# Kernel optimization log

Measured on AMD Instinct MI355X. Metric: run time of the kernel, lower is better.

## Reference

```python
import jax, jax.numpy as jnp
import numpy as np

N, E, B = 50000, 1000000, 64
IN, HID, OUT, H, ED = 25, 128, 64, 4, 6
EPS = 1e-5


def gat_layer(x, src, dst, ea, W, att_s, att_d, We, att_e, bias, heads, ch):
    """PyG GATConv with edge features and self-loops (fill_value='mean').
    x: [N,F_in]; src,dst: [E'] (after self-loops); ea: [E',ED]."""
    n = x.shape[0]
    h = (x @ W).reshape(n, heads, ch)                    # [N,H,C]
    a_src = jnp.einsum('nhc,hc->nh', h, att_s)           # [N,H]
    a_dst = jnp.einsum('nhc,hc->nh', h, att_d)
    e = (ea @ We).reshape(-1, heads, ch)                 # [E',H,C]
    a_edge = jnp.einsum('ehc,hc->eh', e, att_e)          # [E',H]
    alpha = a_src[src] + a_dst[dst] + a_edge
    alpha = jax.nn.leaky_relu(alpha, 0.2)
    # segment softmax over incoming edges of each dst node
    amax = jax.ops.segment_max(alpha, dst, num_segments=n)
    alpha = jnp.exp(alpha - amax[dst])
    denom = jax.ops.segment_sum(alpha, dst, num_segments=n)
    alpha = alpha / (denom[dst] + 1e-16)
    msg = h[src] * alpha[..., None]                      # [E',H,C]
    out = jax.ops.segment_sum(msg, dst, num_segments=n)
    return out.reshape(n, heads * ch) + bias


def batch_norm(x, g, b):
    mu = x.mean(0)
    var = x.var(0)
    return (x - mu) * jax.lax.rsqrt(var + EPS) * g + b


def setup_inputs():
    key = jax.random.key(0)
    ks = jax.random.split(key, 32)
    s = 0.1
    inp = {
        'x': jax.random.normal(ks[0], (N, IN), jnp.float32),
        'edge_index': jax.random.randint(ks[1], (2, E), 0, N, jnp.int32),
        'edge_attr': jax.random.uniform(ks[2], (E, ED), jnp.float32),
        'batch': jnp.sort(jax.random.randint(ks[3], (N,), 0, B, jnp.int32)),
        'repeat_unit_mask': jax.random.randint(ks[4], (N,), 0, 3, jnp.int32),
        'num_graphs': B,
        # layer 1: 25 -> 4 heads x 32
        'W1': jax.random.normal(ks[5], (IN, HID)) * s,
        'att_s1': jax.random.normal(ks[6], (H, HID // H)) * s,
        'att_d1': jax.random.normal(ks[7], (H, HID // H)) * s,
        'We1': jax.random.normal(ks[8], (ED, HID)) * s,
        'att_e1': jax.random.normal(ks[9], (H, HID // H)) * s,
        'b1': jnp.zeros((HID,)),
        'g1': jnp.ones((HID,)), 'be1': jnp.zeros((HID,)),
        # layer 2: 128 -> 4 heads x 32
        'W2': jax.random.normal(ks[10], (HID, HID)) * s,
        'att_s2': jax.random.normal(ks[11], (H, HID // H)) * s,
        'att_d2': jax.random.normal(ks[12], (H, HID // H)) * s,
        'We2': jax.random.normal(ks[13], (ED, HID)) * s,
        'att_e2': jax.random.normal(ks[14], (H, HID // H)) * s,
        'b2': jnp.zeros((HID,)),
        'g2': jnp.ones((HID,)), 'be2': jnp.zeros((HID,)),
        # layer 3: 128 -> 1 head x 64
        'W3': jax.random.normal(ks[15], (HID, OUT)) * s,
        'att_s3': jax.random.normal(ks[16], (1, OUT)) * s,
        'att_d3': jax.random.normal(ks[17], (1, OUT)) * s,
        'We3': jax.random.normal(ks[18], (ED, OUT)) * s,
        'att_e3': jax.random.normal(ks[19], (1, OUT)) * s,
        'b3': jnp.zeros((OUT,)),
    }
    return inp


def reference(x, edge_index, edge_attr, batch, repeat_unit_mask, num_graphs,
              W1, att_s1, att_d1, We1, att_e1, b1, g1, be1,
              W2, att_s2, att_d2, We2, att_e2, b2, g2, be2,
              W3, att_s3, att_d3, We3, att_e3, b3):
    n = x.shape[0]
    # add self-loops once (shared by all layers), edge_attr fill = mean
    loop = jnp.arange(n, dtype=edge_index.dtype)
    src = jnp.concatenate([edge_index[0], loop])
    dst = jnp.concatenate([edge_index[1], loop])
    ea = jnp.concatenate([edge_attr, jnp.broadcast_to(edge_attr.mean(0), (n, edge_attr.shape[1]))], 0)

    h = gat_layer(x, src, dst, ea, W1, att_s1, att_d1, We1, att_e1, b1, H, HID // H)
    h = jax.nn.elu(batch_norm(h, g1, be1))               # dropout = identity (eval)
    h = gat_layer(h, src, dst, ea, W2, att_s2, att_d2, We2, att_e2, b2, H, HID // H)
    h = jax.nn.elu(batch_norm(h, g2, be2))
    h = gat_layer(h, src, dst, ea, W3, att_s3, att_d3, We3, att_e3, b3, 1, OUT)
    h = jax.nn.elu(h)                                    # [N, OUT]

    # GRIN pooling: max over middle repeat-unit atoms (mask == 1) per graph
    mid = (repeat_unit_mask == 1)
    vals = jnp.where(mid[:, None], h, -jnp.inf)
    out = jax.ops.segment_max(vals, batch, num_segments=num_graphs)
    out = jnp.where(jnp.isfinite(out), out, 0.0)         # empty segments -> 0 (torch_scatter default)
    return out
```

## Files before the change

kernel.cpp:

```cpp
#include <hip/hip_runtime.h>
#include <hip/hip_bf16.h>
#include <cstdint>


typedef __attribute__((ext_vector_type(8))) short short8;
typedef __attribute__((ext_vector_type(4))) float floatx4;

__device__ __forceinline__ void atomicMaxFloat(float* addr, float val) {
  if (val >= 0.f) atomicMax((int*)addr, __float_as_int(val));
  else            atomicMin((unsigned int*)addr, __float_as_uint(val));
}

__device__ __forceinline__ float bf2f(unsigned short u) {
  union { uint32_t i; float f; } v; v.i = ((uint32_t)u) << 16; return v.f;
}
__device__ __forceinline__ float u2f(uint32_t u) {
  union { uint32_t i; float f; } v; v.i = u; return v.f;
}
__device__ __forceinline__ unsigned short f2bf(float f) {
  return __bfloat16_as_ushort(__float2bfloat16(f));
}
__device__ __forceinline__ uint32_t pk2(float a, float b) {
  return (uint32_t)f2bf(a) | ((uint32_t)f2bf(b) << 16);
}

#define EA_NBLK 256
#define PCH 4096

__global__ __launch_bounds__(256) void ea_count_kernel(
    const float* __restrict__ ea, float* __restrict__ ea_part,
    const int* __restrict__ dst, int* __restrict__ part,
    int E, int EP, int CB) {
  if (blockIdx.x < EA_NBLK) {
    const int bid = blockIdx.x;
    const int total = 6 * E;
    const int total12 = total / 12;
    float a0 = 0.f, a1 = 0.f, a2 = 0.f, a3 = 0.f, a4 = 0.f, a5 = 0.f;
    const int stride = EA_NBLK * 256;
    for (int i = bid * 256 + threadIdx.x; i < total12; i += stride) {
      const float* b = ea + (size_t)i * 12;
      float4 f0 = *reinterpret_cast<const float4*>(b);
      float4 f1 = *reinterpret_cast<const float4*>(b + 4);
      float4 f2 = *reinterpret_cast<const float4*>(b + 8);
      a0 += f0.x + f1.z;
      a1 += f0.y + f1.w;
      a2 += f0.z + f2.x;
      a3 += f0.w + f2.y;
      a4 += f1.x + f2.z;
      a5 += f1.y + f2.w;
    }
    if (bid == 0 && threadIdx.x == 0) {
      for (int i = total12 * 12; i < total; ++i) {
        int c = i % 6;
        float v = ea[i];
        a0 += (c == 0) ? v : 0.f;
        a1 += (c == 1) ? v : 0.f;
        a2 += (c == 2) ? v : 0.f;
        a3 += (c == 3) ? v : 0.f;
        a4 += (c == 4) ? v : 0.f;
        a5 += (c == 5) ? v : 0.f;
      }
    }
#pragma unroll
    for (int mm = 32; mm >= 1; mm >>= 1) {
      a0 += __shfl_xor(a0, mm); a1 += __shfl_xor(a1, mm);
      a2 += __shfl_xor(a2, mm); a3 += __shfl_xor(a3, mm);
      a4 += __shfl_xor(a4, mm); a5 += __shfl_xor(a5, mm);
    }
    __shared__ float ls[4][6];
    const int lane = threadIdx.x & 63, wv = threadIdx.x >> 6;
    if (lane == 0) {
      ls[wv][0] = a0; ls[wv][1] = a1; ls[wv][2] = a2;
      ls[wv][3] = a3; ls[wv][4] = a4; ls[wv][5] = a5;
    }
    __syncthreads();
    if (threadIdx.x < 6) {
      float s = ls[0][threadIdx.x] + ls[1][threadIdx.x] +
                ls[2][threadIdx.x] + ls[3][threadIdx.x];
      ea_part[threadIdx.x * EA_NBLK + bid] = s;
    }
  } else {
    const int bid = blockIdx.x - EA_NBLK;
    __shared__ int lcnt[256];
    lcnt[threadIdx.x] = 0;
    __syncthreads();
    const int g0 = bid * PCH + threadIdx.x;
#pragma unroll
    for (int j = 0; j < 16; ++j) {
      int g = g0 + j * 256;
      if (g < EP) {
        int d = (g < E) ? dst[g] : (g - E);
        atomicAdd(&lcnt[d >> 8], 1);
      }
    }
    __syncthreads();
    part[(size_t)bid * 256 + threadIdx.x] = lcnt[threadIdx.x];
  }
}

__global__ __launch_bounds__(384) void prep_kernel(
    const float* __restrict__ part, float invE,
    const float* __restrict__ We1, const float* __restrict__ ae1,
    const float* __restrict__ We2, const float* __restrict__ ae2,
    const float* __restrict__ We3, const float* __restrict__ ae3,
    float* __restrict__ we_red, float* __restrict__ ea_mean6) {
  const int tid = threadIdx.x;
  {
    const int ch = tid >> 6, lane = tid & 63;
    float s = part[ch * EA_NBLK + lane] + part[ch * EA_NBLK + lane + 64] +
              part[ch * EA_NBLK + lane + 128] + part[ch * EA_NBLK + lane + 192];
#pragma unroll
    for (int mm = 32; mm >= 1; mm >>= 1) s += __shfl_xor(s, mm);
    if (lane == 0) ea_mean6[ch] = s * invE;
  }
  for (int idx = tid; idx < 72; idx += 384) {
    int l = idx / 24, rem = idx % 24, k = rem / 4, h = rem % 4;
    const float* We; const float* ae; int C, HEADS, F_OUT;
    if (l == 0)      { We = We1; ae = ae1; C = 32; HEADS = 4; F_OUT = 128; }
    else if (l == 1) { We = We2; ae = ae2; C = 32; HEADS = 4; F_OUT = 128; }
    else             { We = We3; ae = ae3; C = 64; HEADS = 1; F_OUT = 64;  }
    float s = 0.f;
    if (h < HEADS)
      for (int c = 0; c < C; ++c) s += We[k * F_OUT + h * C + c] * ae[h * C + c];
    we_red[idx] = s;
  }
}

__global__ __launch_bounds__(256) void bin_scan_kernel(
    int* __restrict__ part, int* __restrict__ btot, int CB, int NB) {
  const int c = blockIdx.x;
  const int tid = threadIdx.x, lane = tid & 63, wv = tid >> 6;
  const int K = (NB + 255) / 256;
  int vals[4];
  int s = 0;
#pragma unroll 4
  for (int k = 0; k < K; ++k) {
    int b = tid * K + k;
    vals[k] = (b < NB) ? part[(size_t)b * 256 + c] : 0;
    s += vals[k];
  }
  int x = s;
#pragma unroll
  for (int off = 1; off < 64; off <<= 1) {
    int t = __shfl_up(x, off);
    if (lane >= off) x += t;
  }
  __shared__ int ws[4];
  if (lane == 63) ws[wv] = x;
  __syncthreads();
  int woff = 0;
#pragma unroll
  for (int k = 0; k < 3; ++k) woff += (k < wv) ? ws[k] : 0;
  int run = woff + x - s;
#pragma unroll 4
  for (int k = 0; k < K; ++k) {
    int b = tid * K + k;
    if (b < NB) part[(size_t)b * 256 + c] = run;
    run += vals[k];
  }
  if (tid == 255) btot[c] = woff + x;
}

__global__ __launch_bounds__(256) void cbase_scan_kernel(
    const int* __restrict__ btot, int* __restrict__ cbase, int CB) {
  const int c = threadIdx.x, lane = c & 63, wv = c >> 6;
  int t = (c < CB) ? btot[c] : 0;
  int x = t;
#pragma unroll
  for (int off = 1; off < 64; off <<= 1) {
    int u = __shfl_up(x, off);
    if (lane >= off) x += u;
  }
  __shared__ int ws[4];
  if (lane == 63) ws[wv] = x;
  __syncthreads();
  int woff = 0;
#pragma unroll
  for (int k = 0; k < 3; ++k) woff += (k < wv) ? ws[k] : 0;
  const int excl = woff + x - t;
  if (c < CB) cbase[c] = excl;
  if (c == CB - 1) cbase[CB] = excl + t;
}

__global__ __launch_bounds__(256) void partition_kernel(
    const int* __restrict__ src, const int* __restrict__ dst,
    const float* __restrict__ ea, const float* __restrict__ ea_mean6,
    const int* __restrict__ part, const int* __restrict__ cbase,
    uint4* __restrict__ ev_tmp, int E, int EP, int CB) {
  __shared__ int loff[256];
  __shared__ int lrk[256];
  lrk[threadIdx.x] = 0;
  if (threadIdx.x < CB)
    loff[threadIdx.x] = cbase[threadIdx.x] +
                        part[(size_t)blockIdx.x * 256 + threadIdx.x];
  __syncthreads();
  const int g0 = blockIdx.x * PCH + threadIdx.x;
#pragma unroll
  for (int j = 0; j < 16; ++j) {
    int g = g0 + j * 256;
    if (g >= EP) continue;
    int d, s;
    float e0, e1, e2, e3, e4, e5;
    if (g < E) {
      d = dst[g]; s = src[g];
      const float* r = ea + (size_t)g * 6;
      float2 f0 = *reinterpret_cast<const float2*>(r);
      float2 f1 = *reinterpret_cast<const float2*>(r + 2);
      float2 f2 = *reinterpret_cast<const float2*>(r + 4);
      e0 = f0.x; e1 = f0.y; e2 = f1.x; e3 = f1.y; e4 = f2.x; e5 = f2.y;
    } else {
      d = g - E; s = d;
      e0 = ea_mean6[0]; e1 = ea_mean6[1]; e2 = ea_mean6[2];
      e3 = ea_mean6[3]; e4 = ea_mean6[4]; e5 = ea_mean6[5];
    }
    const int c = d >> 8;
    const int lr = atomicAdd(&lrk[c], 1);
    uint4 o;
    o.x = (uint32_t)s | ((uint32_t)d << 16);
    o.y = pk2(e0, e1);
    o.z = pk2(e2, e3);
    o.w = pk2(e4, e5);
    ev_tmp[loff[c] + lr] = o;
  }
}

__global__ __launch_bounds__(512) void fine_csr_kernel(
    const uint4* __restrict__ ev_tmp, const int* __restrict__ cbase,
    uint4* __restrict__ ev, int* __restrict__ row_ptr,
    int nN, int CB, int EP) {
  __shared__ int lcnt[256];
  __shared__ int lexcl[256];
  __shared__ int lrk[256];
  __shared__ int ws[4];
  const int tid = threadIdx.x;
  const int c = blockIdx.x;
  if (tid < 256) { lcnt[tid] = 0; lrk[tid] = 0; }
  __syncthreads();
  const int e0 = cbase[c], e1 = cbase[c + 1];
  for (int p = e0 + tid; p < e1; p += 512) {
    uint4 e = ev_tmp[p];
    atomicAdd(&lcnt[(e.x >> 16) & 255], 1);
  }
  __syncthreads();
  const int lane = tid & 63, wv = tid >> 6;
  int v = 0, x = 0;
  if (tid < 256) {
    v = lcnt[tid];
    x = v;
#pragma unroll
    for (int off = 1; off < 64; off <<= 1) {
      int t = __shfl_up(x, off);
      if (lane >= off) x += t;
    }
    if (lane == 63) ws[wv] = x;
  }
  __syncthreads();
  if (tid < 256) {
    int woff = 0;
#pragma unroll
    for (int k = 0; k < 3; ++k) woff += (k < wv) ? ws[k] : 0;
    const int ex = woff + x - v;
    lexcl[tid] = ex;
    const int node = (c << 8) + tid;
    if (node < nN) row_ptr[node] = e0 + ex;
    if (c == CB - 1 && tid == 0) row_ptr[nN] = EP;
  }
  __syncthreads();
  for (int p = e0 + tid; p < e1; p += 512) {
    uint4 e = ev_tmp[p];
    const int li = (int)((e.x >> 16) & 255);
    const int pos = e0 + lexcl[li] + atomicAdd(&lrk[li], 1);
    ev[pos] = e;
  }
}

__global__ __launch_bounds__(256) void pack_conv_kernel(
    const float* __restrict__ W1, const float* __restrict__ W2,
    const float* __restrict__ W3, __hip_bfloat16* __restrict__ wp,
    const float* __restrict__ x, __hip_bfloat16* __restrict__ xb, int nN) {
  int idx = blockIdx.x * 256 + threadIdx.x;
  if (idx < 28672) {
    const float* W; int F_IN, F_OUT, KC, rem;
    if (idx < 4096)       { W = W1; F_IN = 25;  F_OUT = 128; KC = 1; rem = idx; }
    else if (idx < 20480) { W = W2; F_IN = 128; F_OUT = 128; KC = 4; rem = idx - 4096; }
    else                  { W = W3; F_IN = 128; F_OUT = 64;  KC = 4; rem = idx - 20480; }
    int ct = rem / (KC * 512);
    int r2 = rem % (KC * 512);
    int kc = r2 / 512;
    int li = r2 % 512;
    int lane = li >> 3, j = li & 7;
    int k = kc * 32 + ((lane >> 4) << 3) + j;
    int col = ct * 16 + (lane & 15);
    float v = (k < F_IN) ? W[(size_t)k * F_OUT + col] : 0.f;
    wp[idx] = __float2bfloat16(v);
  } else {
    int i = idx - 28672;
    if (i < nN * 32) {
      int n = i >> 5, k = i & 31;
      xb[i] = __float2bfloat16(k < 25 ? x[(size_t)n * 25 + k] : 0.f);
    }
  }
}

#define BN_NBLK 256
__global__ __launch_bounds__(256) void bn_stats_kernel(
    const __hip_bfloat16* __restrict__ x, float* __restrict__ part, int nN) {
  const int c8 = threadIdx.x & 15;
  const int slot = threadIdx.x >> 4;
  float s[8], s2[8];
#pragma unroll
  for (int j = 0; j < 8; ++j) { s[j] = 0.f; s2[j] = 0.f; }
  for (int n = blockIdx.x * 16 + slot; n < nN; n += BN_NBLK * 16) {
    short8 v = *reinterpret_cast<const short8*>(x + (size_t)n * 128 + c8 * 8);
#pragma unroll
    for (int j = 0; j < 8; ++j) {
      float f = bf2f((unsigned short)v[j]);
      s[j] += f; s2[j] += f * f;
    }
  }
#pragma unroll
  for (int j = 0; j < 8; ++j) {
    s[j]  += __shfl_xor(s[j], 16);  s[j]  += __shfl_xor(s[j], 32);
    s2[j] += __shfl_xor(s2[j], 16); s2[j] += __shfl_xor(s2[j], 32);
  }
  __shared__ float ls[4][256];
  const int lane = threadIdx.x & 63, wv = threadIdx.x >> 6;
  if (lane < 16) {
#pragma unroll
    for (int j = 0; j < 8; ++j) {
      ls[wv][c8 * 8 + j] = s[j];
      ls[wv][128 + c8 * 8 + j] = s2[j];
    }
  }
  __syncthreads();
  const int i = threadIdx.x;
  part[(size_t)blockIdx.x * 256 + i] = ls[0][i] + ls[1][i] + ls[2][i] + ls[3][i];
}

__global__ __launch_bounds__(256) void bn_finalize_kernel(
    const float* __restrict__ part,
    const float* __restrict__ g, const float* __restrict__ b,
    float* __restrict__ scale, float* __restrict__ shift, float invN) {
  const int i = threadIdx.x;
  float v0 = 0.f, v1 = 0.f, v2 = 0.f, v3 = 0.f;
  for (int bk = 0; bk < BN_NBLK; bk += 4) {
    v0 += part[(size_t)bk * 256 + i];
    v1 += part[(size_t)(bk + 1) * 256 + i];
    v2 += part[(size_t)(bk + 2) * 256 + i];
    v3 += part[(size_t)(bk + 3) * 256 + i];
  }
  __shared__ float sums[256];
  sums[i] = (v0 + v1) + (v2 + v3);
  __syncthreads();
  if (i < 128) {
    float mu = sums[i] * invN;
    float var = sums[128 + i] * invN - mu * mu;
    float sc = rsqrtf(var + 1e-5f) * g[i];
    scale[i] = sc;
    shift[i] = b[i] - mu * sc;
  }
}

template<int K, int NT, int KC, int HEADS, bool BN>
__global__ __launch_bounds__(256) void feat_mfma_kernel(
    const void* __restrict__ xin, const __hip_bfloat16* __restrict__ wp,
    const float* __restrict__ att_s, const float* __restrict__ att_d,
    const float* __restrict__ bsc, const float* __restrict__ bsh,
    __hip_bfloat16* __restrict__ hout, float* __restrict__ a_src,
    float* __restrict__ a_dst, int nN) {
  constexpr int F_OUT = NT * 16;
  __shared__ __hip_bfloat16 hs[64][F_OUT + 4];
  const int tid = threadIdx.x;
  const int lane = tid & 63, w = tid >> 6;
  const int base = blockIdx.x * 64;

  const int nd = min(base + (w << 4) + (lane & 15), nN - 1);
  short8 a[KC];
  if constexpr (!BN) {
    const __hip_bfloat16* xb = (const __hip_bfloat16*)xin;
#pragma unroll
    for (int kc = 0; kc < KC; ++kc)
      a[kc] = *reinterpret_cast<const short8*>(
          xb + (size_t)nd * K + kc * 32 + ((lane >> 4) << 3));
  } else {
    const __hip_bfloat16* xb = (const __hip_bfloat16*)xin;
#pragma unroll
    for (int kc = 0; kc < KC; ++kc) {
      const int kb = kc * 32 + ((lane >> 4) << 3);
      short8 xv = *reinterpret_cast<const short8*>(xb + (size_t)nd * K + kb);
      float4 s0 = *reinterpret_cast<const float4*>(bsc + kb);
      float4 s1 = *reinterpret_cast<const float4*>(bsc + kb + 4);
      float4 t0 = *reinterpret_cast<const float4*>(bsh + kb);
      float4 t1 = *reinterpret_cast<const float4*>(bsh + kb + 4);
      float scj[8] = {s0.x, s0.y, s0.z, s0.w, s1.x, s1.y, s1.z, s1.w};
      float shj[8] = {t0.x, t0.y, t0.z, t0.w, t1.x, t1.y, t1.z, t1.w};
      union { short8 sv; unsigned short us[8]; } u;
#pragma unroll
      for (int j = 0; j < 8; ++j) {
        float v = bf2f((unsigned short)xv[j]) * scj[j] + shj[j];
        float t = (v > 0.f) ? v : (__expf(v) - 1.f);
        u.us[j] = f2bf(t);
      }
      a[kc] = u.sv;
    }
  }

  floatx4 acc[NT];
#pragma unroll
  for (int ct = 0; ct < NT; ++ct) acc[ct] = (floatx4){0.f, 0.f, 0.f, 0.f};

#pragma unroll
  for (int ct = 0; ct < NT; ++ct) {
#pragma unroll
    for (int kc = 0; kc < KC; ++kc) {
      short8 b = *reinterpret_cast<const short8*>(wp + ((size_t)(ct * KC + kc) * 64 + lane) * 8);
      acc[ct] = __builtin_amdgcn_mfma_f32_16x16x32_bf16(a[kc], b, acc[ct], 0, 0, 0);
    }
  }

#pragma unroll
  for (int ct = 0; ct < NT; ++ct) {
#pragma unroll
    for (int r = 0; r < 4; ++r) {
      int row = (w << 4) + ((lane >> 4) << 2) + r;
      hs[row][ct * 16 + (lane & 15)] = __float2bfloat16(acc[ct][r]);
    }
  }
  __syncthreads();

  {
    constexpr int PART = F_OUT / 4;
    const int ln = tid >> 2, q = tid & 3;
    const int n = base + ln;
    float ssum = 0.f, dsum = 0.f;
#pragma unroll
    for (int j = 0; j < PART; ++j) {
      int c = q * PART + j;
      float hv = bf2f(__bfloat16_as_ushort(hs[ln][c]));
      ssum += hv * att_s[c];
      dsum += hv * att_d[c];
    }
    if constexpr (HEADS == 4) {
      if (n < nN) {
        a_src[(size_t)n * 4 + q] = ssum;
        a_dst[(size_t)n * 4 + q] = dsum;
      }
    } else {
      ssum += __shfl_xor(ssum, 1); ssum += __shfl_xor(ssum, 2);
      dsum += __shfl_xor(dsum, 1); dsum += __shfl_xor(dsum, 2);
      if (n < nN && q == 0) { a_src[n] = ssum; a_dst[n] = dsum; }
    }
  }

  constexpr int C4 = F_OUT / 4;
  for (int idx = tid; idx < 64 * C4; idx += 256) {
    int row = idx / C4, cw = idx % C4;
    int n = base + row;
    if (n < nN)
      *reinterpret_cast<uint2*>(hout + (size_t)n * F_OUT + cw * 4) =
          *reinterpret_cast<const uint2*>(&hs[row][cw * 4]);
  }
}

template<int HEADS, int C>
__global__ __launch_bounds__(256) void agg_kernel(
    const int* __restrict__ row_ptr, const uint4* __restrict__ ev,
    const float* __restrict__ we_red,
    const float* __restrict__ a_src, const float* __restrict__ a_dst,
    const __hip_bfloat16* __restrict__ hfeat,
    const float* __restrict__ bias, __hip_bfloat16* __restrict__ out, int nN) {
  const int lane = threadIdx.x & 63;
  const int n = blockIdx.x * 4 + (threadIdx.x >> 6);
  if (n >= nN) return;
  const int r0 = row_ptr[n], r1 = row_ptr[n + 1];

#define FMA2(k, ha, hb)                                                   \
  acc2[k].x += wA * u2f((ha) << 16) + wB * u2f((hb) << 16);               \
  acc2[k].y += wA * u2f((ha) & 0xffff0000u) + wB * u2f((hb) & 0xffff0000u);

  if constexpr (HEADS == 4) {
    const int es = lane >> 4;
    const int L = lane & 15;
    const int fo = L << 3;
    const int h = L >> 2;
    const int q1 = L & 1;
    const float wr0 = we_red[0 * 4 + h], wr1 = we_red[1 * 4 + h];
    const float wr2 = we_red[2 * 4 + h], wr3 = we_red[3 * 4 + h];
    const float wr4 = we_red[4 * 4 + h], wr5 = we_red[5 * 4 + h];
    const float adh = a_dst[(size_t)n * 4 + h];
    float2 acc2[4];
#pragma unroll
    for (int j = 0; j < 4; ++j) acc2[j] = make_float2(0.f, 0.f);
    float dsum = 0.f;
    int p = r0 + es;
    uint4 wa = make_uint4(0, 0, 0, 0), wb = make_uint4(0, 0, 0, 0);
    if (p < r1) wa = ev[p];
    if (p + 4 < r1) wb = ev[p + 4];
    for (; p < r1; p += 8) {
      const int sA = (int)(wa.x & 0xffffu);
      const int sB = (int)(wb.x & 0xffffu);
      uint4 hA = *reinterpret_cast<const uint4*>(hfeat + (size_t)sA * 128 + fo);
      uint4 hB = *reinterpret_cast<const uint4*>(hfeat + (size_t)sB * 128 + fo);
      const uint32_t ry = q1 ? wb.y : wa.y;
      const uint32_t rz = q1 ? wb.z : wa.z;
      const uint32_t rw = q1 ? wb.w : wa.w;
      const int ss = q1 ? sB : sA;
      const float asS = a_src[(size_t)ss * 4 + h];
      const int pn = p + 8;
      uint4 wa_n = make_uint4(0, 0, 0, 0), wb_n = make_uint4(0, 0, 0, 0);
      if (pn < r1) wa_n = ev[pn];
      if (pn + 4 < r1) wb_n = ev[pn + 4];
      float ae = u2f(ry << 16) * wr0 + u2f(ry & 0xffff0000u) * wr1 +
                 u2f(rz << 16) * wr2 + u2f(rz & 0xffff0000u) * wr3 +
                 u2f(rw << 16) * wr4 + u2f(rw & 0xffff0000u) * wr5;
      float a = asS + adh + ae;
      a = (a >= 0.f) ? a : 0.2f * a;
      const float wme = __expf(a);
      const float wot = __shfl_xor(wme, 1);
      const float wA = q1 ? wot : wme;
      float wB = q1 ? wme : wot;
      wB = (p + 4 < r1) ? wB : 0.f;
      dsum += wA + wB;
      FMA2(0, hA.x, hB.x); FMA2(1, hA.y, hB.y);
      FMA2(2, hA.z, hB.z); FMA2(3, hA.w, hB.w);
      wa = wa_n; wb = wb_n;
    }
#pragma unroll
    for (int j = 0; j < 4; ++j) {
      acc2[j].x += __shfl_xor(acc2[j].x, 16);
      acc2[j].y += __shfl_xor(acc2[j].y, 16);
      acc2[j].x += __shfl_xor(acc2[j].x, 32);
      acc2[j].y += __shfl_xor(acc2[j].y, 32);
    }
    dsum += __shfl_xor(dsum, 16);
    dsum += __shfl_xor(dsum, 32);
    if (lane < 16) {
      const float invd = 1.f / (dsum + 1e-16f);
      float4 b0 = *reinterpret_cast<const float4*>(bias + fo);
      float4 b1 = *reinterpret_cast<const float4*>(bias + fo + 4);
      uint4 o;
      o.x = pk2(acc2[0].x * invd + b0.x, acc2[0].y * invd + b0.y);
      o.y = pk2(acc2[1].x * invd + b0.z, acc2[1].y * invd + b0.w);
      o.z = pk2(acc2[2].x * invd + b1.x, acc2[2].y * invd + b1.y);
      o.w = pk2(acc2[3].x * invd + b1.z, acc2[3].y * invd + b1.w);
      *reinterpret_cast<uint4*>(out + (size_t)n * 128 + fo) = o;
    }
  } else {
    const int es = lane >> 3;
    const int L = lane & 7;
    const int fo = L << 3;
    const int q1 = L & 1;
    const float wr0 = we_red[0], wr1 = we_red[4], wr2 = we_red[8];
    const float wr3 = we_red[12], wr4 = we_red[16], wr5 = we_red[20];
    const float adh = a_dst[n];
    float2 acc2[4];
#pragma unroll
    for (int j = 0; j < 4; ++j) acc2[j] = make_float2(0.f, 0.f);
    float dsum = 0.f;
    int p = r0 + es;
    uint4 wa = make_uint4(0, 0, 0, 0), wb = make_uint4(0, 0, 0, 0);
    if (p < r1) wa = ev[p];
    if (p + 8 < r1) wb = ev[p + 8];
    for (; p < r1; p += 16) {
      const int sA = (int)(wa.x & 0xffffu);
      const int sB = (int)(wb.x & 0xffffu);
      uint4 hA = *reinterpret_cast<const uint4*>(hfeat + (size_t)sA * 64 + fo);
      uint4 hB = *reinterpret_cast<const uint4*>(hfeat + (size_t)sB * 64 + fo);
      const uint32_t ry = q1 ? wb.y : wa.y;
      const uint32_t rz = q1 ? wb.z : wa.z;
      const uint32_t rw = q1 ? wb.w : wa.w;
      const int ss = q1 ? sB : sA;
      const float asS = a_src[ss];
      const int pn = p + 16;
      uint4 wa_n = make_uint4(0, 0, 0, 0), wb_n = make_uint4(0, 0, 0, 0);
      if (pn < r1) wa_n = ev[pn];
      if (pn + 8 < r1) wb_n = ev[pn + 8];
      float ae = u2f(ry << 16) * wr0 + u2f(ry & 0xffff0000u) * wr1 +
                 u2f(rz << 16) * wr2 + u2f(rz & 0xffff0000u) * wr3 +
                 u2f(rw << 16) * wr4 + u2f(rw & 0xffff0000u) * wr5;
      float a = asS + adh + ae;
      a = (a >= 0.f) ? a : 0.2f * a;
      const float wme = __expf(a);
      const float wot = __shfl_xor(wme, 1);
      const float wA = q1 ? wot : wme;
      float wB = q1 ? wme : wot;
      wB = (p + 8 < r1) ? wB : 0.f;
      dsum += wA + wB;
      FMA2(0, hA.x, hB.x); FMA2(1, hA.y, hB.y);
      FMA2(2, hA.z, hB.z); FMA2(3, hA.w, hB.w);
      wa = wa_n; wb = wb_n;
    }
#pragma unroll
    for (int j = 0; j < 4; ++j) {
      acc2[j].x += __shfl_xor(acc2[j].x, 8);
      acc2[j].y += __shfl_xor(acc2[j].y, 8);
      acc2[j].x += __shfl_xor(acc2[j].x, 16);
      acc2[j].y += __shfl_xor(acc2[j].y, 16);
      acc2[j].x += __shfl_xor(acc2[j].x, 32);
      acc2[j].y += __shfl_xor(acc2[j].y, 32);
    }
    dsum += __shfl_xor(dsum, 8);
    dsum += __shfl_xor(dsum, 16);
    dsum += __shfl_xor(dsum, 32);
    if (lane < 8) {
      const float invd = 1.f / (dsum + 1e-16f);
      float4 b0 = *reinterpret_cast<const float4*>(bias + fo);
      float4 b1 = *reinterpret_cast<const float4*>(bias + fo + 4);
      uint4 o;
      o.x = pk2(acc2[0].x * invd + b0.x, acc2[0].y * invd + b0.y);
      o.y = pk2(acc2[1].x * invd + b0.z, acc2[1].y * invd + b0.w);
      o.z = pk2(acc2[2].x * invd + b1.x, acc2[2].y * invd + b1.y);
      o.w = pk2(acc2[3].x * invd + b1.z, acc2[3].y * invd + b1.w);
      *reinterpret_cast<uint4*>(out + (size_t)n * 64 + fo) = o;
    }
  }
#undef FMA2
}

__global__ __launch_bounds__(64) void pool_kernel(
    const __hip_bfloat16* __restrict__ h3, const int* __restrict__ batch,
    const int* __restrict__ mask, float* __restrict__ out, int nN) {
  const int c = threadIdx.x;
  int n0 = blockIdx.x * 32;
  int n1 = min(n0 + 32, nN);
  float cur = -INFINITY;
  int curb = -1;
  for (int n = n0; n < n1; ++n) {
    if (mask[n] != 1) continue;
    int b = batch[n];
    if (b != curb) {
      if (curb >= 0) atomicMaxFloat(&out[curb * 64 + c], cur);
      curb = b; cur = -INFINITY;
    }
    float v = bf2f(__bfloat16_as_ushort(h3[(size_t)n * 64 + c]));
    v = (v > 0.f) ? v : (__expf(v) - 1.f);
    cur = fmaxf(cur, v);
  }
  if (curb >= 0) atomicMaxFloat(&out[curb * 64 + c], cur);
}

__global__ __launch_bounds__(256) void fixup_kernel(float* __restrict__ out, int sz) {
  int i = blockIdx.x * 256 + threadIdx.x;
  if (i >= sz) return;
  float v = out[i];
  if (!(v > -INFINITY && v < INFINITY)) out[i] = 0.f;
}

extern "C" void kernel_launch(void* const* d_in, const int* in_sizes, int n_in,
                              void* d_out, int out_size, void* d_ws, size_t ws_size,
                              hipStream_t stream) {
  (void)n_in; (void)ws_size;
  const float* x     = (const float*)d_in[0];
  const int*   ei    = (const int*)d_in[1];
  const float* ea    = (const float*)d_in[2];
  const int*   batch = (const int*)d_in[3];
  const int*   mask  = (const int*)d_in[4];
  const float* W1 = (const float*)d_in[6];
  const float* as1 = (const float*)d_in[7];
  const float* ad1 = (const float*)d_in[8];
  const float* We1 = (const float*)d_in[9];
  const float* ae1 = (const float*)d_in[10];
  const float* b1 = (const float*)d_in[11];
  const float* g1 = (const float*)d_in[12];
  const float* be1 = (const float*)d_in[13];
  const float* W2 = (const float*)d_in[14];
  const float* as2 = (const float*)d_in[15];
  const float* ad2 = (const float*)d_in[16];
  const float* We2 = (const float*)d_in[17];
  const float* ae2 = (const float*)d_in[18];
  const float* b2 = (const float*)d_in[19];
  const float* g2 = (const float*)d_in[20];
  const float* be2 = (const float*)d_in[21];
  const float* W3 = (const float*)d_in[22];
  const float* as3 = (const float*)d_in[23];
  const float* ad3 = (const float*)d_in[24];
  const float* We3 = (const float*)d_in[25];
  const float* ae3 = (const float*)d_in[26];
  const float* b3 = (const float*)d_in[27];

  const int N = in_sizes[0] / 25;
  const int E = in_sizes[1] / 2;
  const int EP = E + N;
  const int* srcI = ei;
  const int* dstI = ei + E;

  const int CB = (N + 255) >> 8;
  const int nb = (EP + PCH - 1) / PCH;

  char* w = (char*)d_ws;
  auto alloc = [&](size_t bytes) { char* p = w; w += (bytes + 255) / 256 * 256; return p; };
  float* ea_part = (float*)alloc(6 * EA_NBLK * 4);
  float* we_red  = (float*)alloc(3 * 6 * 4 * 4);
  float* ea_m6   = (float*)alloc(6 * 4);
  int*   row_ptr = (int*)alloc((size_t)(N + 1) * 4);
  int*   part    = (int*)alloc((size_t)nb * 256 * 4);
  int*   btot    = (int*)alloc((size_t)CB * 4);
  int*   cbase   = (int*)alloc((size_t)(CB + 1) * 4);
  uint4* ev      = (uint4*)alloc((size_t)EP * 16);
  float* a_srcb  = (float*)alloc((size_t)N * 4 * 4);
  float* a_dstb  = (float*)alloc((size_t)N * 4 * 4);
  __hip_bfloat16* hbuf = (__hip_bfloat16*)alloc((size_t)N * 128 * 2);
  size_t obsz = (size_t)N * 128 * 2;
  size_t evsz = (size_t)EP * 16;
  __hip_bfloat16* obuf = (__hip_bfloat16*)alloc(obsz > evsz ? obsz : evsz);
  __hip_bfloat16* x1b  = (__hip_bfloat16*)alloc((size_t)N * 32 * 2);
  __hip_bfloat16* wp   = (__hip_bfloat16*)alloc(28672 * 2);
  float* bn_part = (float*)alloc((size_t)BN_NBLK * 256 * 4);
  float* bn_sc   = (float*)alloc(128 * 4);
  float* bn_sh   = (float*)alloc(128 * 4);
  uint4* ev_tmp  = (uint4*)obuf;

  hipMemsetAsync(d_out, 0xFF, (size_t)out_size * 4, stream);
  ea_count_kernel<<<EA_NBLK + nb, 256, 0, stream>>>(ea, ea_part, dstI, part, E, EP, CB);
  prep_kernel<<<1, 384, 0, stream>>>(ea_part, 1.f / (float)E, We1, ae1, We2, ae2, We3, ae3,
                                     we_red, ea_m6);
  bin_scan_kernel<<<CB, 256, 0, stream>>>(part, btot, CB, nb);
  cbase_scan_kernel<<<1, 256, 0, stream>>>(btot, cbase, CB);
  partition_kernel<<<nb, 256, 0, stream>>>(srcI, dstI, ea, ea_m6, part, cbase,
                                           ev_tmp, E, EP, CB);
  fine_csr_kernel<<<CB, 512, 0, stream>>>(ev_tmp, cbase, ev, row_ptr, N, CB, EP);
  pack_conv_kernel<<<(28672 + N * 32 + 255) / 256, 256, 0, stream>>>(
      W1, W2, W3, wp, x, x1b, N);

  const int gMf = (N + 63) / 64;
  const int gAgg = (N + 3) / 4;

  feat_mfma_kernel<32, 8, 1, 4, false><<<gMf, 256, 0, stream>>>(
      x1b, wp, as1, ad1, nullptr, nullptr, hbuf, a_srcb, a_dstb, N);
  agg_kernel<4, 32><<<gAgg, 256, 0, stream>>>(row_ptr, ev, we_red + 0,
                                              a_srcb, a_dstb, hbuf, b1, obuf, N);
  bn_stats_kernel<<<BN_NBLK, 256, 0, stream>>>(obuf, bn_part, N);
  bn_finalize_kernel<<<1, 256, 0, stream>>>(bn_part, g1, be1, bn_sc, bn_sh, 1.f / (float)N);

  feat_mfma_kernel<128, 8, 4, 4, true><<<gMf, 256, 0, stream>>>(
      obuf, wp + 4096, as2, ad2, bn_sc, bn_sh, hbuf, a_srcb, a_dstb, N);
  agg_kernel<4, 32><<<gAgg, 256, 0, stream>>>(row_ptr, ev, we_red + 24,
                                              a_srcb, a_dstb, hbuf, b2, obuf, N);
  bn_stats_kernel<<<BN_NBLK, 256, 0, stream>>>(obuf, bn_part, N);
  bn_finalize_kernel<<<1, 256, 0, stream>>>(bn_part, g2, be2, bn_sc, bn_sh, 1.f / (float)N);

  feat_mfma_kernel<128, 4, 4, 1, true><<<gMf, 256, 0, stream>>>(
      obuf, wp + 20480, as3, ad3, bn_sc, bn_sh, hbuf, a_srcb, a_dstb, N);
  agg_kernel<1, 64><<<gAgg, 256, 0, stream>>>(row_ptr, ev, we_red + 48,
                                              a_srcb, a_dstb, hbuf, b3, obuf, N);

  pool_kernel<<<(N + 31) / 32, 64, 0, stream>>>(obuf, batch, mask, (float*)d_out, N);
  fixup_kernel<<<(out_size + 255) / 256, 256, 0, stream>>>((float*)d_out, out_size);
}
```

Before: 249.4 us.

## Split 4-head aggregation into two feature-half slices with interleaved block mapping

The 4-head aggregation kernel now splits each node's 128-wide feature row into two 64-wide slices handled by separate blocks. Blocks are interleaved so that both slices of the same node group run close together in time. Each wave uses 8 lanes per edge and 8 edges in flight, like the single-head path. The aim is to raise edge-level parallelism per wave and shrink the gathered footprint per block to improve cache locality. The cost is that edge records, a_src lookups and the exp/softmax work are repeated for each slice, doubling that part of the traffic.

```diff
diff --git a/kernel.cpp b/kernel.cpp
--- a/kernel.cpp
+++ b/kernel.cpp
@@ -462,8 +462,99 @@
   }
 }
 
-template<int HEADS, int C>
-__global__ __launch_bounds__(256) void agg_kernel(
+#define FMA2(k, ha, hb)                                                   \
+  acc2[k].x += wA * u2f((ha) << 16) + wB * u2f((hb) << 16);               \
+  acc2[k].y += wA * u2f((ha) & 0xffff0000u) + wB * u2f((hb) & 0xffff0000u);
+
+__global__ __launch_bounds__(256) void agg4s_kernel(
+    const int* __restrict__ row_ptr, const uint4* __restrict__ ev,
+    const float* __restrict__ we_red,
+    const float* __restrict__ a_src, const float* __restrict__ a_dst,
+    const __hip_bfloat16* __restrict__ hfeat,
+    const float* __restrict__ bias, __hip_bfloat16* __restrict__ out,
+    int nN, int ng) {
+  const int bid = blockIdx.x;
+  const int r = bid & 7, g = bid >> 3;
+  const int slice = r >> 2;
+  const int grp = g * 4 + (r & 3);
+  if (grp >= ng) return;
+  const int lane = threadIdx.x & 63;
+  const int n = grp * 4 + (threadIdx.x >> 6);
+  if (n >= nN) return;
+  const int r0 = row_ptr[n], r1 = row_ptr[n + 1];
+
+  const int es = lane >> 3;
+  const int L = lane & 7;
+  const int fo = slice * 64 + (L << 3);
+  const int h = fo >> 5;
+  const int q1 = L & 1;
+  const float wr0 = we_red[0 * 4 + h], wr1 = we_red[1 * 4 + h];
+  const float wr2 = we_red[2 * 4 + h], wr3 = we_red[3 * 4 + h];
+  const float wr4 = we_red[4 * 4 + h], wr5 = we_red[5 * 4 + h];
+  const float adh = a_dst[(size_t)n * 4 + h];
+  float2 acc2[4];
+#pragma unroll
+  for (int j = 0; j < 4; ++j) acc2[j] = make_float2(0.f, 0.f);
+  float dsum = 0.f;
+  int p = r0 + es;
+  uint4 wa = make_uint4(0, 0, 0, 0), wb = make_uint4(0, 0, 0, 0);
+  if (p < r1) wa = ev[p];
+  if (p + 8 < r1) wb = ev[p + 8];
+  for (; p < r1; p += 16) {
+    const int sA = (int)(wa.x & 0xffffu);
+    const int sB = (int)(wb.x & 0xffffu);
+    uint4 hA = *reinterpret_cast<const uint4*>(hfeat + (size_t)sA * 128 + fo);
+    uint4 hB = *reinterpret_cast<const uint4*>(hfeat + (size_t)sB * 128 + fo);
+    const uint32_t ry = q1 ? wb.y : wa.y;
+    const uint32_t rz = q1 ? wb.z : wa.z;
+    const uint32_t rw = q1 ? wb.w : wa.w;
+    const int ss = q1 ? sB : sA;
+    const float asS = a_src[(size_t)ss * 4 + h];
+    const int pn = p + 16;
+    uint4 wa_n = make_uint4(0, 0, 0, 0), wb_n = make_uint4(0, 0, 0, 0);
+    if (pn < r1) wa_n = ev[pn];
+    if (pn + 8 < r1) wb_n = ev[pn + 8];
+    float ae = u2f(ry << 16) * wr0 + u2f(ry & 0xffff0000u) * wr1 +
+               u2f(rz << 16) * wr2 + u2f(rz & 0xffff0000u) * wr3 +
+               u2f(rw << 16) * wr4 + u2f(rw & 0xffff0000u) * wr5;
+    float a = asS + adh + ae;
+    a = (a >= 0.f) ? a : 0.2f * a;
+    const float wme = __expf(a);
+    const float wot = __shfl_xor(wme, 1);
+    const float wA = q1 ? wot : wme;
+    float wB = q1 ? wme : wot;
+    wB = (p + 8 < r1) ? wB : 0.f;
+    dsum += wA + wB;
+    FMA2(0, hA.x, hB.x); FMA2(1, hA.y, hB.y);
+    FMA2(2, hA.z, hB.z); FMA2(3, hA.w, hB.w);
+    wa = wa_n; wb = wb_n;
+  }
+#pragma unroll
+  for (int j = 0; j < 4; ++j) {
+    acc2[j].x += __shfl_xor(acc2[j].x, 8);
+    acc2[j].y += __shfl_xor(acc2[j].y, 8);
+    acc2[j].x += __shfl_xor(acc2[j].x, 16);
+    acc2[j].y += __shfl_xor(acc2[j].y, 16);
+    acc2[j].x += __shfl_xor(acc2[j].x, 32);
+    acc2[j].y += __shfl_xor(acc2[j].y, 32);
+  }
+  dsum += __shfl_xor(dsum, 8);
+  dsum += __shfl_xor(dsum, 16);
+  dsum += __shfl_xor(dsum, 32);
+  if (lane < 8) {
+    const float invd = 1.f / (dsum + 1e-16f);
+    float4 b0 = *reinterpret_cast<const float4*>(bias + fo);
+    float4 b1 = *reinterpret_cast<const float4*>(bias + fo + 4);
+    uint4 o;
+    o.x = pk2(acc2[0].x * invd + b0.x, acc2[0].y * invd + b0.y);
+    o.y = pk2(acc2[1].x * invd + b0.z, acc2[1].y * invd + b0.w);
+    o.z = pk2(acc2[2].x * invd + b1.x, acc2[2].y * invd + b1.y);
+    o.w = pk2(acc2[3].x * invd + b1.z, acc2[3].y * invd + b1.w);
+    *reinterpret_cast<uint4*>(out + (size_t)n * 128 + fo) = o;
+  }
+}
+
+__global__ __launch_bounds__(256) void agg1_kernel(
     const int* __restrict__ row_ptr, const uint4* __restrict__ ev,
     const float* __restrict__ we_red,
     const float* __restrict__ a_src, const float* __restrict__ a_dst,
@@ -474,148 +565,75 @@
   if (n >= nN) return;
   const int r0 = row_ptr[n], r1 = row_ptr[n + 1];
 
-#define FMA2(k, ha, hb)                                                   \
-  acc2[k].x += wA * u2f((ha) << 16) + wB * u2f((hb) << 16);               \
-  acc2[k].y += wA * u2f((ha) & 0xffff0000u) + wB * u2f((hb) & 0xffff0000u);
-
-  if constexpr (HEADS == 4) {
-    const int es = lane >> 4;
-    const int L = lane & 15;
-    const int fo = L << 3;
-    const int h = L >> 2;
-    const int q1 = L & 1;
-    const float wr0 = we_red[0 * 4 + h], wr1 = we_red[1 * 4 + h];
-    const float wr2 = we_red[2 * 4 + h], wr3 = we_red[3 * 4 + h];
-    const float wr4 = we_red[4 * 4 + h], wr5 = we_red[5 * 4 + h];
-    const float adh = a_dst[(size_t)n * 4 + h];
-    float2 acc2[4];
-#pragma unroll
-    for (int j = 0; j < 4; ++j) acc2[j] = make_float2(0.f, 0.f);
-    float dsum = 0.f;
-    int p = r0 + es;
-    uint4 wa = make_uint4(0, 0, 0, 0), wb = make_uint4(0, 0, 0, 0);
-    if (p < r1) wa = ev[p];
-    if (p + 4 < r1) wb = ev[p + 4];
-    for (; p < r1; p += 8) {
-      const int sA = (int)(wa.x & 0xffffu);
-      const int sB = (int)(wb.x & 0xffffu);
-      uint4 hA = *reinterpret_cast<const uint4*>(hfeat + (size_t)sA * 128 + fo);
-      uint4 hB = *reinterpret_cast<const uint4*>(hfeat + (size_t)sB * 128 + fo);
-      const uint32_t ry = q1 ? wb.y : wa.y;
-      const uint32_t rz = q1 ? wb.z : wa.z;
-      const uint32_t rw = q1 ? wb.w : wa.w;
-      const int ss = q1 ? sB : sA;
-      const float asS = a_src[(size_t)ss * 4 + h];
-      const int pn = p + 8;
-      uint4 wa_n = make_uint4(0, 0, 0, 0), wb_n = make_uint4(0, 0, 0, 0);
-      if (pn < r1) wa_n = ev[pn];
-      if (pn + 4 < r1) wb_n = ev[pn + 4];
-      float ae = u2f(ry << 16) * wr0 + u2f(ry & 0xffff0000u) * wr1 +
-                 u2f(rz << 16) * wr2 + u2f(rz & 0xffff0000u) * wr3 +
-                 u2f(rw << 16) * wr4 + u2f(rw & 0xffff0000u) * wr5;
-      float a = asS + adh + ae;
-      a = (a >= 0.f) ? a : 0.2f * a;
-      const float wme = __expf(a);
-      const float wot = __shfl_xor(wme, 1);
-      const float wA = q1 ? wot : wme;
-      float wB = q1 ? wme : wot;
-      wB = (p + 4 < r1) ? wB : 0.f;
-      dsum += wA + wB;
-      FMA2(0, hA.x, hB.x); FMA2(1, hA.y, hB.y);
-      FMA2(2, hA.z, hB.z); FMA2(3, hA.w, hB.w);
-      wa = wa_n; wb = wb_n;
-    }
-#pragma unroll
-    for (int j = 0; j < 4; ++j) {
-      acc2[j].x += __shfl_xor(acc2[j].x, 16);
-      acc2[j].y += __shfl_xor(acc2[j].y, 16);
-      acc2[j].x += __shfl_xor(acc2[j].x, 32);
-      acc2[j].y += __shfl_xor(acc2[j].y, 32);
-    }
-    dsum += __shfl_xor(dsum, 16);
-    dsum += __shfl_xor(dsum, 32);
-    if (lane < 16) {
-      const float invd = 1.f / (dsum + 1e-16f);
-      float4 b0 = *reinterpret_cast<const float4*>(bias + fo);
-      float4 b1 = *reinterpret_cast<const float4*>(bias + fo + 4);
-      uint4 o;
-      o.x = pk2(acc2[0].x * invd + b0.x, acc2[0].y * invd + b0.y);
-      o.y = pk2(acc2[1].x * invd + b0.z, acc2[1].y * invd + b0.w);
-      o.z = pk2(acc2[2].x * invd + b1.x, acc2[2].y * invd + b1.y);
-      o.w = pk2(acc2[3].x * invd + b1.z, acc2[3].y * invd + b1.w);
-      *reinterpret_cast<uint4*>(out + (size_t)n * 128 + fo) = o;
-    }
-  } else {
-    const int es = lane >> 3;
-    const int L = lane & 7;
-    const int fo = L << 3;
-    const int q1 = L & 1;
-    const float wr0 = we_red[0], wr1 = we_red[4], wr2 = we_red[8];
-    const float wr3 = we_red[12], wr4 = we_red[16], wr5 = we_red[20];
-    const float adh = a_dst[n];
-    float2 acc2[4];
-#pragma unroll
-    for (int j = 0; j < 4; ++j) acc2[j] = make_float2(0.f, 0.f);
-    float dsum = 0.f;
-    int p = r0 + es;
-    uint4 wa = make_uint4(0, 0, 0, 0), wb = make_uint4(0, 0, 0, 0);
-    if (p < r1) wa = ev[p];
-    if (p + 8 < r1) wb = ev[p + 8];
-    for (; p < r1; p += 16) {
-      const int sA = (int)(wa.x & 0xffffu);
-      const int sB = (int)(wb.x & 0xffffu);
-      uint4 hA = *reinterpret_cast<const uint4*>(hfeat + (size_t)sA * 64 + fo);
-      uint4 hB = *reinterpret_cast<const uint4*>(hfeat + (size_t)sB * 64 + fo);
-      const uint32_t ry = q1 ? wb.y : wa.y;
-      const uint32_t rz = q1 ? wb.z : wa.z;
-      const uint32_t rw = q1 ? wb.w : wa.w;
-      const int ss = q1 ? sB : sA;
-      const float asS = a_src[ss];
-      const int pn = p + 16;
-      uint4 wa_n = make_uint4(0, 0, 0, 0), wb_n = make_uint4(0, 0, 0, 0);
-      if (pn < r1) wa_n = ev[pn];
-      if (pn + 8 < r1) wb_n = ev[pn + 8];
-      float ae = u2f(ry << 16) * wr0 + u2f(ry & 0xffff0000u) * wr1 +
-                 u2f(rz << 16) * wr2 + u2f(rz & 0xffff0000u) * wr3 +
-                 u2f(rw << 16) * wr4 + u2f(rw & 0xffff0000u) * wr5;
-      float a = asS + adh + ae;
-      a = (a >= 0.f) ? a : 0.2f * a;
-      const float wme = __expf(a);
-      const float wot = __shfl_xor(wme, 1);
-      const float wA = q1 ? wot : wme;
-      float wB = q1 ? wme : wot;
-      wB = (p + 8 < r1) ? wB : 0.f;
-      dsum += wA + wB;
-      FMA2(0, hA.x, hB.x); FMA2(1, hA.y, hB.y);
-      FMA2(2, hA.z, hB.z); FMA2(3, hA.w, hB.w);
-      wa = wa_n; wb = wb_n;
-    }
-#pragma unroll
-    for (int j = 0; j < 4; ++j) {
-      acc2[j].x += __shfl_xor(acc2[j].x, 8);
-      acc2[j].y += __shfl_xor(acc2[j].y, 8);
-      acc2[j].x += __shfl_xor(acc2[j].x, 16);
-      acc2[j].y += __shfl_xor(acc2[j].y, 16);
-      acc2[j].x += __shfl_xor(acc2[j].x, 32);
-      acc2[j].y += __shfl_xor(acc2[j].y, 32);
-    }
-    dsum += __shfl_xor(dsum, 8);
-    dsum += __shfl_xor(dsum, 16);
-    dsum += __shfl_xor(dsum, 32);
-    if (lane < 8) {
-      const float invd = 1.f / (dsum + 1e-16f);
-      float4 b0 = *reinterpret_cast<const float4*>(bias + fo);
-      float4 b1 = *reinterpret_cast<const float4*>(bias + fo + 4);
-      uint4 o;
-      o.x = pk2(acc2[0].x * invd + b0.x, acc2[0].y * invd + b0.y);
-      o.y = pk2(acc2[1].x * invd + b0.z, acc2[1].y * invd + b0.w);
-      o.z = pk2(acc2[2].x * invd + b1.x, acc2[2].y * invd + b1.y);
-      o.w = pk2(acc2[3].x * invd + b1.z, acc2[3].y * invd + b1.w);
-      *reinterpret_cast<uint4*>(out + (size_t)n * 64 + fo) = o;
-    }
-  }
+  const int es = lane >> 3;
+  const int L = lane & 7;
+  const int fo = L << 3;
+  const int q1 = L & 1;
+  const float wr0 = we_red[0], wr1 = we_red[4], wr2 = we_red[8];
+  const float wr3 = we_red[12], wr4 = we_red[16], wr5 = we_red[20];
+  const float adh = a_dst[n];
+  float2 acc2[4];
+#pragma unroll
+  for (int j = 0; j < 4; ++j) acc2[j] = make_float2(0.f, 0.f);
+  float dsum = 0.f;
+  int p = r0 + es;
+  uint4 wa = make_uint4(0, 0, 0, 0), wb = make_uint4(0, 0, 0, 0);
+  if (p < r1) wa = ev[p];
+  if (p + 8 < r1) wb = ev[p + 8];
+  for (; p < r1; p += 16) {
+    const int sA = (int)(wa.x & 0xffffu);
+    const int sB = (int)(wb.x & 0xffffu);
+    uint4 hA = *reinterpret_cast<const uint4*>(hfeat + (size_t)sA * 64 + fo);
+    uint4 hB = *reinterpret_cast<const uint4*>(hfeat + (size_t)sB * 64 + fo);
+    const uint32_t ry = q1 ? wb.y : wa.y;
+    const uint32_t rz = q1 ? wb.z : wa.z;
+    const uint32_t rw = q1 ? wb.w : wa.w;
+    const int ss = q1 ? sB : sA;
+    const float asS = a_src[ss];
+    const int pn = p + 16;
+    uint4 wa_n = make_uint4(0, 0, 0, 0), wb_n = make_uint4(0, 0, 0, 0);
+    if (pn < r1) wa_n = ev[pn];
+    if (pn + 8 < r1) wb_n = ev[pn + 8];
+    float ae = u2f(ry << 16) * wr0 + u2f(ry & 0xffff0000u) * wr1 +
+               u2f(rz << 16) * wr2 + u2f(rz & 0xffff0000u) * wr3 +
+               u2f(rw << 16) * wr4 + u2f(rw & 0xffff0000u) * wr5;
+    float a = asS + adh + ae;
+    a = (a >= 0.f) ? a : 0.2f * a;
+    const float wme = __expf(a);
+    const float wot = __shfl_xor(wme, 1);
+    const float wA = q1 ? wot : wme;
+    float wB = q1 ? wme : wot;
+    wB = (p + 8 < r1) ? wB : 0.f;
+    dsum += wA + wB;
+    FMA2(0, hA.x, hB.x); FMA2(1, hA.y, hB.y);
+    FMA2(2, hA.z, hB.z); FMA2(3, hA.w, hB.w);
+    wa = wa_n; wb = wb_n;
+  }
+#pragma unroll
+  for (int j = 0; j < 4; ++j) {
+    acc2[j].x += __shfl_xor(acc2[j].x, 8);
+    acc2[j].y += __shfl_xor(acc2[j].y, 8);
+    acc2[j].x += __shfl_xor(acc2[j].x, 16);
+    acc2[j].y += __shfl_xor(acc2[j].y, 16);
+    acc2[j].x += __shfl_xor(acc2[j].x, 32);
+    acc2[j].y += __shfl_xor(acc2[j].y, 32);
+  }
+  dsum += __shfl_xor(dsum, 8);
+  dsum += __shfl_xor(dsum, 16);
+  dsum += __shfl_xor(dsum, 32);
+  if (lane < 8) {
+    const float invd = 1.f / (dsum + 1e-16f);
+    float4 b0 = *reinterpret_cast<const float4*>(bias + fo);
+    float4 b1 = *reinterpret_cast<const float4*>(bias + fo + 4);
+    uint4 o;
+    o.x = pk2(acc2[0].x * invd + b0.x, acc2[0].y * invd + b0.y);
+    o.y = pk2(acc2[1].x * invd + b0.z, acc2[1].y * invd + b0.w);
+    o.z = pk2(acc2[2].x * invd + b1.x, acc2[2].y * invd + b1.y);
+    o.w = pk2(acc2[3].x * invd + b1.z, acc2[3].y * invd + b1.w);
+    *reinterpret_cast<uint4*>(out + (size_t)n * 64 + fo) = o;
+  }
+}
 #undef FMA2
-}
 
 __global__ __launch_bounds__(64) void pool_kernel(
     const __hip_bfloat16* __restrict__ h3, const int* __restrict__ batch,
@@ -723,26 +741,28 @@
       W1, W2, W3, wp, x, x1b, N);
 
   const int gMf = (N + 63) / 64;
-  const int gAgg = (N + 3) / 4;
+  const int ng = (N + 3) / 4;
+  const int gAggS = 8 * ((ng + 3) / 4);
+  const int gAgg = ng;
 
   feat_mfma_kernel<32, 8, 1, 4, false><<<gMf, 256, 0, stream>>>(
       x1b, wp, as1, ad1, nullptr, nullptr, hbuf, a_srcb, a_dstb, N);
-  agg_kernel<4, 32><<<gAgg, 256, 0, stream>>>(row_ptr, ev, we_red + 0,
-                                              a_srcb, a_dstb, hbuf, b1, obuf, N);
+  agg4s_kernel<<<gAggS, 256, 0, stream>>>(row_ptr, ev, we_red + 0,
+                                          a_srcb, a_dstb, hbuf, b1, obuf, N, ng);
   bn_stats_kernel<<<BN_NBLK, 256, 0, stream>>>(obuf, bn_part, N);
   bn_finalize_kernel<<<1, 256, 0, stream>>>(bn_part, g1, be1, bn_sc, bn_sh, 1.f / (float)N);
 
   feat_mfma_kernel<128, 8, 4, 4, true><<<gMf, 256, 0, stream>>>(
       obuf, wp + 4096, as2, ad2, bn_sc, bn_sh, hbuf, a_srcb, a_dstb, N);
-  agg_kernel<4, 32><<<gAgg, 256, 0, stream>>>(row_ptr, ev, we_red + 24,
-                                              a_srcb, a_dstb, hbuf, b2, obuf, N);
+  agg4s_kernel<<<gAggS, 256, 0, stream>>>(row_ptr, ev, we_red + 24,
+                                          a_srcb, a_dstb, hbuf, b2, obuf, N, ng);
   bn_stats_kernel<<<BN_NBLK, 256, 0, stream>>>(obuf, bn_part, N);
   bn_finalize_kernel<<<1, 256, 0, stream>>>(bn_part, g2, be2, bn_sc, bn_sh, 1.f / (float)N);
 
   feat_mfma_kernel<128, 4, 4, 1, true><<<gMf, 256, 0, stream>>>(
       obuf, wp + 20480, as3, ad3, bn_sc, bn_sh, hbuf, a_srcb, a_dstb, N);
-  agg_kernel<1, 64><<<gAgg, 256, 0, stream>>>(row_ptr, ev, we_red + 48,
-                                              a_srcb, a_dstb, hbuf, b3, obuf, N);
+  agg1_kernel<<<gAgg, 256, 0, stream>>>(row_ptr, ev, we_red + 48,
+                                        a_srcb, a_dstb, hbuf, b3, obuf, N);
 
   pool_kernel<<<(N + 31) / 32, 64, 0, stream>>>(obuf, batch, mask, (float*)d_out, N);
   fixup_kernel<<<(out_size + 255) / 256, 256, 0, stream>>>((float*)d_out, out_size);
```

Measured after the change: 270.8 us. 8.6% more time.
